# Performance work log

Measured on AMD Instinct MI355X. Metric: run time of the kernel, lower is better.

The kernel has to match this reference:

```python
import jax, jax.numpy as jnp
import numpy as np
from jax import lax

MAXIMIZE = True  # matches init_kwargs

def setup_inputs() -> dict:
    key = jax.random.key(0)
    cost_matrix = jax.random.normal(key, (1024, 16384), dtype=jnp.float32)
    return {"cost_matrix": cost_matrix}

def _greedy_assign(cost_matrix):
    n_rows, n_cols = cost_matrix.shape
    n_assign = min(n_rows, n_cols)
    # maximize=True -> keep costs as-is; else negate (matches torch module)
    costs = cost_matrix if MAXIMIZE else -cost_matrix
    neg_inf = jnp.array(-jnp.inf, dtype=costs.dtype)

    def step(carry, _):
        row_used, col_used = carry  # bool [n_rows], bool [n_cols]
        mask = row_used[:, None] | col_used[None, :]
        masked = jnp.where(mask, neg_inf, costs)
        flat = jnp.argmax(masked)  # row-major flat argmax, same as torch reshape(-1).argmax()
        r = flat // n_cols
        c = flat % n_cols
        row_used = row_used.at[r].set(True)
        col_used = col_used.at[c].set(True)
        return (row_used, col_used), (r, c)

    init = (jnp.zeros(n_rows, dtype=bool), jnp.zeros(n_cols, dtype=bool))
    _, (rows, cols) = lax.scan(step, init, None, length=n_assign)
    rows = rows.astype(jnp.int64) if rows.dtype != jnp.int64 else rows
    cols = cols.astype(jnp.int64) if cols.dtype != jnp.int64 else cols
    sort_idx = jnp.argsort(rows)
    return rows[sort_idx], cols[sort_idx]

def reference(cost_matrix):
    row_ind, col_ind = _greedy_assign(cost_matrix)
    return (row_ind, col_ind)
```

## Files before the change

kernel.cpp:

```cpp
#include <hip/hip_runtime.h>
#include <stdint.h>

#define NROWS 1024
#define NCOLS 16384
#define NRB 64
#define NCB 16
#define TROWS 16
#define NROUNDS 2
#define NBLK (NRB * NCB)

#define NLEAF 64
#define LEAFSZ (NBLK / NLEAF)

typedef unsigned long long u64;
typedef unsigned int u32;

__device__ u64 g_rowpart[NCB * NROWS];
__device__ u64 g_colpart[(size_t)NRB * NCOLS];
__device__ u64 g_rowbest[NROWS];
__device__ int g_col_used[NCOLS];
__device__ int g_row_assigned[NROWS];
__device__ int g_rem[2][NROWS];
__device__ int g_cnt[NROUNDS + 1];

__device__ int g_bar_leaf[NLEAF * 32];
__device__ int g_bar_root;
__device__ int g_bar_gen;

__device__ __forceinline__ u64 ald64(const u64* p) {
    return __hip_atomic_load((u64*)p, __ATOMIC_RELAXED, __HIP_MEMORY_SCOPE_AGENT);
}
__device__ __forceinline__ void ast64(u64* p, u64 v) {
    __hip_atomic_store(p, v, __ATOMIC_RELAXED, __HIP_MEMORY_SCOPE_AGENT);
}
__device__ __forceinline__ int ald32(const int* p) {
    return __hip_atomic_load((int*)p, __ATOMIC_RELAXED, __HIP_MEMORY_SCOPE_AGENT);
}
__device__ __forceinline__ void ast32(int* p, int v) {
    __hip_atomic_store(p, v, __ATOMIC_RELAXED, __HIP_MEMORY_SCOPE_AGENT);
}
__device__ __forceinline__ int aadd32(int* p, int v) {
    return __hip_atomic_fetch_add(p, v, __ATOMIC_RELAXED, __HIP_MEMORY_SCOPE_AGENT);
}

__device__ __forceinline__ void grid_barrier(int bid, int tid) {
    asm volatile("s_waitcnt vmcnt(0)" ::: "memory");
    __syncthreads();
    if (tid == 0) {
        int gen = ald32(&g_bar_gen);
        asm volatile("s_waitcnt vmcnt(0)" ::: "memory");
        int leaf = (bid & (NLEAF - 1)) * 32;
        int v = aadd32(&g_bar_leaf[leaf], 1);
        if ((v & (LEAFSZ - 1)) == LEAFSZ - 1) {
            int u = aadd32(&g_bar_root, 1);
            if ((u & (NLEAF - 1)) == NLEAF - 1) {
                aadd32(&g_bar_gen, 1);
            }
        }
        while (ald32(&g_bar_gen) == gen) {
            __builtin_amdgcn_s_sleep(8);
        }
    }
    __syncthreads();
    asm volatile("" ::: "memory");
}

__device__ __forceinline__ u32 fsort(float x) {
    u32 u = __float_as_uint(x);
    return u ^ ((u32)((int)u >> 31) | 0x80000000u);
}

__device__ __forceinline__ u64 wave_reduce_max(u64 v) {
    for (int off = 32; off; off >>= 1) {
        u64 o = __shfl_down(v, off);
        if (o > v) v = o;
    }
    return v;
}

__device__ __forceinline__ u64 block_reduce_max(u64 v, u64* s_part) {
    v = wave_reduce_max(v);
    int wave = threadIdx.x >> 6;
    if ((threadIdx.x & 63) == 0) s_part[wave] = v;
    __syncthreads();
    u64 b = s_part[0];
    for (int w = 1; w < 4; w++) if (s_part[w] > b) b = s_part[w];
    __syncthreads();
    return b;
}

__device__ __forceinline__ void scan_row(float4 v, int r, int c0,
                                         u64& b0, u64& b1, u64& b2, u64& b3,
                                         u64& m) {
    u32 rk = (u32)(NROWS - 1 - r);
    u64 k0 = ((u64)fsort(v.x) << 32) | rk; if (k0 > b0) b0 = k0;
    u64 k1 = ((u64)fsort(v.y) << 32) | rk; if (k1 > b1) b1 = k1;
    u64 k2 = ((u64)fsort(v.z) << 32) | rk; if (k2 > b2) b2 = k2;
    u64 k3 = ((u64)fsort(v.w) << 32) | rk; if (k3 > b3) b3 = k3;
    u64 m0 = ((u64)fsort(v.x) << 32) | (u32)(NCOLS - 1 - (c0 + 0));
    u64 m1 = ((u64)fsort(v.y) << 32) | (u32)(NCOLS - 1 - (c0 + 1));
    u64 m2 = ((u64)fsort(v.z) << 32) | (u32)(NCOLS - 1 - (c0 + 2));
    u64 m3 = ((u64)fsort(v.w) << 32) | (u32)(NCOLS - 1 - (c0 + 3));
    m = m0; if (m1 > m) m = m1; if (m2 > m) m = m2; if (m3 > m) m = m3;
}

__device__ __forceinline__ void phase_scan(const float* __restrict__ cost,
                                           int fb, int tid,
                                           u64 (*s_cand)[256],
                                           u64 (*s_p2)[17]) {
    const int cb = fb & (NCB - 1);
    const int rb = fb >> 4;
    const int cbase = cb * 1024;
    const int r0 = rb * TROWS;
    const int c0 = cbase + tid * 4;

    if (rb == 0) {
        ast64((u64*)(g_col_used + cbase) + tid * 2 + 0, 0ULL);
        ast64((u64*)(g_col_used + cbase) + tid * 2 + 1, 0ULL);
        if (cb == 0 && tid <= NROUNDS) ast32(&g_cnt[tid], 0);
    }

    u64 b0 = 0, b1 = 0, b2 = 0, b3 = 0;
    for (int half = 0; half < 2; ++half) {
        const int rbase = r0 + half * 8;
        for (int g = 0; g < 8; g += 4) {
            const float* base = cost + (size_t)(rbase + g) * NCOLS + c0;
            float4 v0 = *(const float4*)(base);
            float4 v1 = *(const float4*)(base + NCOLS);
            float4 v2 = *(const float4*)(base + 2 * NCOLS);
            float4 v3 = *(const float4*)(base + 3 * NCOLS);
            u64 m0, m1, m2, m3;
            scan_row(v0, rbase + g + 0, c0, b0, b1, b2, b3, m0);
            scan_row(v1, rbase + g + 1, c0, b0, b1, b2, b3, m1);
            scan_row(v2, rbase + g + 2, c0, b0, b1, b2, b3, m2);
            scan_row(v3, rbase + g + 3, c0, b0, b1, b2, b3, m3);
            s_cand[g + 0][tid] = m0;
            s_cand[g + 1][tid] = m1;
            s_cand[g + 2][tid] = m2;
            s_cand[g + 3][tid] = m3;
        }
        __syncthreads();
        if (tid < 128) {
            int r = tid >> 4, j = tid & 15;
            u64 m = s_cand[r][j];
            #pragma unroll
            for (int i = 1; i < 16; i++) {
                u64 o = s_cand[r][j + 16 * i];
                if (o > m) m = o;
            }
            s_p2[half * 8 + r][j] = m;
        }
        __syncthreads();
    }
    size_t cp = (size_t)rb * NCOLS + c0;
    ast64(&g_colpart[cp + 0], b0);
    ast64(&g_colpart[cp + 1], b1);
    ast64(&g_colpart[cp + 2], b2);
    ast64(&g_colpart[cp + 3], b3);
    if (tid < TROWS) {
        u64 m = s_p2[tid][0];
        #pragma unroll
        for (int i = 1; i < 16; i++) {
            u64 o = s_p2[tid][i];
            if (o > m) m = o;
        }
        ast64(&g_rowpart[cb * NROWS + (r0 + tid)], m);
    }
}

__device__ __forceinline__ void phase_commit(int* __restrict__ out, int r, int lane) {
    u64 v = ald64(&g_rowpart[(lane & 15) * NROWS + r]);
    u64 key = wave_reduce_max(v);
    key = __shfl(key, 0);
    int c = NCOLS - 1 - (int)(key & 0xFFFFFFFFu);

    u64 cp = ald64(&g_colpart[(size_t)lane * NCOLS + c]);
    u64 colmax = wave_reduce_max(cp);

    if (lane == 0) {
        ast64(&g_rowbest[r], key);
        out[r] = r;
        u64 mk = (key & 0xFFFFFFFF00000000ULL) | (u32)(NROWS - 1 - r);
        if (colmax == mk) {
            ast32(&g_col_used[c], 1);
            ast32(&g_row_assigned[r], 1);
            out[NROWS + r] = c;
        } else {
            ast32(&g_row_assigned[r], 0);
            int p = aadd32(&g_cnt[0], 1);
            ast32(&g_rem[0][p], r);
        }
    }
}

__device__ __forceinline__ void phase_round(const float* __restrict__ cost,
                                            int* __restrict__ out, int t, int r,
                                            int tid, u64* s_part) {
    if (ald32(&g_row_assigned[r])) return;

    u64 key = ald64(&g_rowbest[r]);
    int c = NCOLS - 1 - (int)(key & 0xFFFFFFFFu);
    if (ald32(&g_col_used[c])) {
        u64 best = 0ULL;
        const float4* row = (const float4*)(cost + (size_t)r * NCOLS);
        const u64* used = (const u64*)g_col_used;
        for (int k = tid; k < NCOLS / 4; k += 256) {
            float4 v = row[k];
            u64 w0 = ald64(&used[k * 2 + 0]);
            u64 w1 = ald64(&used[k * 2 + 1]);
            int c0 = k * 4;
            if (!(u32)w0)         { u64 kk = ((u64)fsort(v.x) << 32) | (u32)(NCOLS - 1 - (c0 + 0)); if (kk > best) best = kk; }
            if (!(u32)(w0 >> 32)) { u64 kk = ((u64)fsort(v.y) << 32) | (u32)(NCOLS - 1 - (c0 + 1)); if (kk > best) best = kk; }
            if (!(u32)w1)         { u64 kk = ((u64)fsort(v.z) << 32) | (u32)(NCOLS - 1 - (c0 + 2)); if (kk > best) best = kk; }
            if (!(u32)(w1 >> 32)) { u64 kk = ((u64)fsort(v.w) << 32) | (u32)(NCOLS - 1 - (c0 + 3)); if (kk > best) best = kk; }
        }
        key = block_reduce_max(best, s_part);
        if (tid == 0) ast64(&g_rowbest[r], key);
        c = NCOLS - 1 - (int)(key & 0xFFFFFFFFu);
    }

    int n = ald32(&g_cnt[t]);
    const int* list = g_rem[t & 1];
    u64 mine = (key & 0xFFFFFFFF00000000ULL) | (u32)(NROWS - 1 - r);
    u64 mx = 0ULL;
    for (int j = tid; j < n; j += 256) {
        int rj = ald32(&list[j]);
        if (rj != r) {
            float x = cost[(size_t)rj * NCOLS + c];
            u64 kj = ((u64)fsort(x) << 32) | (u32)(NROWS - 1 - rj);
            if (kj > mx) mx = kj;
        }
    }
    mx = block_reduce_max(mx, s_part);
    if (tid == 0) {
        if (mine > mx) {
            ast32(&g_col_used[c], 1);
            ast32(&g_row_assigned[r], 1);
            out[NROWS + r] = c;
        } else {
            int p = aadd32(&g_cnt[t + 1], 1);
            ast32(&g_rem[(t + 1) & 1][p], r);
        }
    }
}

__device__ __forceinline__ void phase_finish(const float* __restrict__ cost,
                                             int* __restrict__ out, int tid,
                                             int (*s_rem)[NROWS], u64* s_part,
                                             int* s_nn) {
    if (tid == 0) s_nn[0] = ald32(&g_cnt[NROUNDS]);
    __syncthreads();
    int n = s_nn[0];
    if (n == 0) return;
    for (int i = tid; i < n; i += 256) s_rem[0][i] = ald32(&g_rem[NROUNDS & 1][i]);
    __syncthreads();
    int cur = 0;
    while (n > 0) {
        for (int i = 0; i < n; i++) {
            int r = s_rem[cur][i];
            u64 key = ald64(&g_rowbest[r]);
            int c = NCOLS - 1 - (int)(key & 0xFFFFFFFFu);
            if (ald32(&g_col_used[c])) {
                u64 best = 0ULL;
                const float4* row = (const float4*)(cost + (size_t)r * NCOLS);
                const u64* used = (const u64*)g_col_used;
                for (int k = tid; k < NCOLS / 4; k += 256) {
                    float4 v = row[k];
                    u64 w0 = ald64(&used[k * 2 + 0]);
                    u64 w1 = ald64(&used[k * 2 + 1]);
                    int c0 = k * 4;
                    if (!(u32)w0)         { u64 kk = ((u64)fsort(v.x) << 32) | (u32)(NCOLS - 1 - (c0 + 0)); if (kk > best) best = kk; }
                    if (!(u32)(w0 >> 32)) { u64 kk = ((u64)fsort(v.y) << 32) | (u32)(NCOLS - 1 - (c0 + 1)); if (kk > best) best = kk; }
                    if (!(u32)w1)         { u64 kk = ((u64)fsort(v.z) << 32) | (u32)(NCOLS - 1 - (c0 + 2)); if (kk > best) best = kk; }
                    if (!(u32)(w1 >> 32)) { u64 kk = ((u64)fsort(v.w) << 32) | (u32)(NCOLS - 1 - (c0 + 3)); if (kk > best) best = kk; }
                }
                u64 m = block_reduce_max(best, s_part);
                if (tid == 0) ast64(&g_rowbest[r], m);
            }
        }
        __syncthreads();
        if (tid == 0) s_nn[1] = 0;
        __syncthreads();
        for (int base = 0; base < n; base += 256) {
            bool win = false; int myr = -1, myc = -1;
            if (base + tid < n) {
                int r = s_rem[cur][base + tid];
                u64 key = ald64(&g_rowbest[r]);
                int c = NCOLS - 1 - (int)(key & 0xFFFFFFFFu);
                u64 mine = (key & 0xFFFFFFFF00000000ULL) | (u32)(NROWS - 1 - r);
                win = true;
                for (int j = 0; j < n; j++) {
                    int rj = s_rem[cur][j];
                    if (rj == r) continue;
                    float x = cost[(size_t)rj * NCOLS + c];
                    u64 kj = ((u64)fsort(x) << 32) | (u32)(NROWS - 1 - rj);
                    if (kj > mine) { win = false; break; }
                }
                myr = r; myc = c;
            }
            if (win) {
                ast32(&g_col_used[myc], 1);
                ast32(&g_row_assigned[myr], 1);
                out[NROWS + myr] = myc;
            }
            if (base + tid < n && !win) {
                int p = atomicAdd(&s_nn[1], 1);
                s_rem[cur ^ 1][p] = myr;
            }
        }
        __syncthreads();
        n = s_nn[1];
        cur ^= 1;
        __syncthreads();
    }
}

__global__ void __launch_bounds__(256, 4)
k_fused(const float* __restrict__ cost, int* __restrict__ out) {
    __shared__ u64 s_cand[8][256];
    __shared__ u64 s_p2[TROWS][17];
    __shared__ u64 s_part[4];
    __shared__ int s_nn[2];
    const int bid = blockIdx.x;
    const int tid = threadIdx.x;

    phase_scan(cost, bid, tid, s_cand, s_p2);
    grid_barrier(bid, tid);

    if (tid < 64) phase_commit(out, bid, tid);
    grid_barrier(bid, tid);

    phase_round(cost, out, 0, bid, tid, s_part);
    grid_barrier(bid, tid);

    phase_round(cost, out, 1, bid, tid, s_part);
    grid_barrier(bid, tid);

    if (bid == 0)
        phase_finish(cost, out, tid,
                     reinterpret_cast<int(*)[NROWS]>(&s_cand[0][0]),
                     s_part, s_nn);
}

extern "C" void kernel_launch(void* const* d_in, const int* in_sizes, int n_in,
                              void* d_out, int out_size, void* d_ws, size_t ws_size,
                              hipStream_t stream) {
    const float* cost = (const float*)d_in[0];
    int* out = (int*)d_out;
    k_fused<<<dim3(NBLK), dim3(256), 0, stream>>>(cost, out);
}
```

Measured before the change: 141.6 us.

## Replace partial row/column max buffers with global atomic max reductions

Instead of writing per-block partial column and row maxima to large global arrays and reducing them with a wave in the commit phase, each block does 64-bit atomic max directly into compact per-column and per-row best arrays. The commit phase then needs only a single thread doing two loads per row. The arrays are reset to zero at the end of the kernel by spare blocks so the next launch starts clean. This trades a large partial-array write and read for atomic contention, and it relies on the arrays being zero before the first launch and on the end-of-kernel reset completing. The shared candidate buffer is also padded to 257 columns.

```diff
diff --git a/kernel.cpp b/kernel.cpp
--- a/kernel.cpp
+++ b/kernel.cpp
@@ -15,8 +15,8 @@
 typedef unsigned long long u64;
 typedef unsigned int u32;
 
-__device__ u64 g_rowpart[NCB * NROWS];
-__device__ u64 g_colpart[(size_t)NRB * NCOLS];
+__device__ u64 g_colbest[NCOLS];
+__device__ u64 g_rowmax[NROWS];
 __device__ u64 g_rowbest[NROWS];
 __device__ int g_col_used[NCOLS];
 __device__ int g_row_assigned[NROWS];
@@ -32,6 +32,9 @@
 }
 __device__ __forceinline__ void ast64(u64* p, u64 v) {
     __hip_atomic_store(p, v, __ATOMIC_RELAXED, __HIP_MEMORY_SCOPE_AGENT);
+}
+__device__ __forceinline__ void amax64(u64* p, u64 v) {
+    (void)__hip_atomic_fetch_max(p, v, __ATOMIC_RELAXED, __HIP_MEMORY_SCOPE_AGENT);
 }
 __device__ __forceinline__ int ald32(const int* p) {
     return __hip_atomic_load((int*)p, __ATOMIC_RELAXED, __HIP_MEMORY_SCOPE_AGENT);
@@ -106,7 +109,7 @@
 
 __device__ __forceinline__ void phase_scan(const float* __restrict__ cost,
                                            int fb, int tid,
-                                           u64 (*s_cand)[256],
+                                           u64 (*s_cand)[257],
                                            u64 (*s_p2)[17]) {
     const int cb = fb & (NCB - 1);
     const int rb = fb >> 4;
@@ -152,11 +155,10 @@
         }
         __syncthreads();
     }
-    size_t cp = (size_t)rb * NCOLS + c0;
-    ast64(&g_colpart[cp + 0], b0);
-    ast64(&g_colpart[cp + 1], b1);
-    ast64(&g_colpart[cp + 2], b2);
-    ast64(&g_colpart[cp + 3], b3);
+    amax64(&g_colbest[c0 + 0], b0);
+    amax64(&g_colbest[c0 + 1], b1);
+    amax64(&g_colbest[c0 + 2], b2);
+    amax64(&g_colbest[c0 + 3], b3);
     if (tid < TROWS) {
         u64 m = s_p2[tid][0];
         #pragma unroll
@@ -164,32 +166,26 @@
             u64 o = s_p2[tid][i];
             if (o > m) m = o;
         }
-        ast64(&g_rowpart[cb * NROWS + (r0 + tid)], m);
-    }
-}
-
-__device__ __forceinline__ void phase_commit(int* __restrict__ out, int r, int lane) {
-    u64 v = ald64(&g_rowpart[(lane & 15) * NROWS + r]);
-    u64 key = wave_reduce_max(v);
-    key = __shfl(key, 0);
+        amax64(&g_rowmax[r0 + tid], m);
+    }
+}
+
+__device__ __forceinline__ void phase_commit(int* __restrict__ out, int r) {
+    u64 key = ald64(&g_rowmax[r]);
     int c = NCOLS - 1 - (int)(key & 0xFFFFFFFFu);
-
-    u64 cp = ald64(&g_colpart[(size_t)lane * NCOLS + c]);
-    u64 colmax = wave_reduce_max(cp);
-
-    if (lane == 0) {
-        ast64(&g_rowbest[r], key);
-        out[r] = r;
-        u64 mk = (key & 0xFFFFFFFF00000000ULL) | (u32)(NROWS - 1 - r);
-        if (colmax == mk) {
-            ast32(&g_col_used[c], 1);
-            ast32(&g_row_assigned[r], 1);
-            out[NROWS + r] = c;
-        } else {
-            ast32(&g_row_assigned[r], 0);
-            int p = aadd32(&g_cnt[0], 1);
-            ast32(&g_rem[0][p], r);
-        }
+    u64 colmax = ald64(&g_colbest[c]);
+
+    ast64(&g_rowbest[r], key);
+    out[r] = r;
+    u64 mk = (key & 0xFFFFFFFF00000000ULL) | (u32)(NROWS - 1 - r);
+    if (colmax == mk) {
+        ast32(&g_col_used[c], 1);
+        ast32(&g_row_assigned[r], 1);
+        out[NROWS + r] = c;
+    } else {
+        ast32(&g_row_assigned[r], 0);
+        int p = aadd32(&g_cnt[0], 1);
+        ast32(&g_rem[0][p], r);
     }
 }
 
@@ -317,7 +313,7 @@
 
 __global__ void __launch_bounds__(256, 4)
 k_fused(const float* __restrict__ cost, int* __restrict__ out) {
-    __shared__ u64 s_cand[8][256];
+    __shared__ u64 s_cand[8][257];
     __shared__ u64 s_p2[TROWS][17];
     __shared__ u64 s_part[4];
     __shared__ int s_nn[2];
@@ -327,7 +323,7 @@
     phase_scan(cost, bid, tid, s_cand, s_p2);
     grid_barrier(bid, tid);
 
-    if (tid < 64) phase_commit(out, bid, tid);
+    if (tid == 0) phase_commit(out, bid);
     grid_barrier(bid, tid);
 
     phase_round(cost, out, 0, bid, tid, s_part);
@@ -336,10 +332,15 @@
     phase_round(cost, out, 1, bid, tid, s_part);
     grid_barrier(bid, tid);
 
-    if (bid == 0)
+    if (bid == 0) {
         phase_finish(cost, out, tid,
                      reinterpret_cast<int(*)[NROWS]>(&s_cand[0][0]),
                      s_part, s_nn);
+    } else if (bid <= 64) {
+        ast64(&g_colbest[(bid - 1) * 256 + tid], 0ULL);
+    } else if (bid <= 68) {
+        ast64(&g_rowmax[(bid - 65) * 256 + tid], 0ULL);
+    }
 }
 
 extern "C" void kernel_launch(void* const* d_in, const int* in_sizes, int n_in,
```

Measured after the change: 150.9 us. +6.6%, slower.
